# Performance work log

Measured on AMD Instinct MI355X. Metric: run time of the kernel, lower is better.

Reference implementation:

```python
import jax, jax.numpy as jnp
import numpy as np

B, N, D_IN, D_OUT = 4, 2048, 1024, 1024

def setup_inputs() -> dict:
    key = jax.random.key(0)
    ks = jax.random.split(key, 7)
    s_in = 1.0 / np.sqrt(D_IN)
    return {
        "X": jax.random.normal(ks[0], (B, N, D_IN), dtype=jnp.float32),
        "Wq": jax.random.uniform(ks[1], (D_IN, D_OUT), jnp.float32, -s_in, s_in),
        "bq": jax.random.uniform(ks[2], (D_OUT,), jnp.float32, -s_in, s_in),
        "Wk": jax.random.uniform(ks[3], (D_IN, D_OUT), jnp.float32, -s_in, s_in),
        "bk": jax.random.uniform(ks[4], (D_OUT,), jnp.float32, -s_in, s_in),
        "Wv": jax.random.uniform(ks[5], (D_IN, D_OUT), jnp.float32, -s_in, s_in),
        "bv": jax.random.uniform(ks[6], (D_OUT,), jnp.float32, -s_in, s_in),
    }

def reference(X, Wq, bq, Wk, bk, Wv, bv):
    # QKV projections: [B,N,D_in] @ [D_in,D_out] -> [B,N,D_out]
    q = jnp.einsum('bnd,de->bne', X, Wq) + bq
    k = jnp.einsum('bnd,de->bne', X, Wk) + bk
    v = jnp.einsum('bnd,de->bne', X, Wv) + bv
    # Unscaled attention (faithful: original has no 1/sqrt(d))
    scores = jnp.einsum('bne,bme->bnm', q, k)  # [B,N,N]
    weights = jax.nn.softmax(scores, axis=-1)
    return jnp.einsum('bnm,bme->bne', weights, v)
```

## Files before the change

kernel.cpp:

```cpp
#include <hip/hip_runtime.h>
#include <hip/hip_bf16.h>
#include <hip/hip_fp16.h>
#include <stdint.h>
#include <math.h>


typedef unsigned short ushort_t;
typedef __attribute__((ext_vector_type(8))) _Float16  f16x8;
typedef __attribute__((ext_vector_type(4))) _Float16  f16x4;
typedef __attribute__((ext_vector_type(4))) float     f32x4;

__device__ __forceinline__ void async_load16(const void* g, void* l) {
  __builtin_amdgcn_global_load_lds(
      (const __attribute__((address_space(1))) void*)g,
      (__attribute__((address_space(3))) void*)l, 16, 0, 0);
}

#define A0OFF 0
#define B0OFF 16384
#define A1OFF 32768
#define B1OFF 49152

template<int SHIFT>
__device__ __forceinline__ void stage_half(const ushort_t* __restrict__ gb,
                                           int k0, int q, ushort_t* lt, int t)
{
#pragma unroll
  for (int j = 0; j < 2; ++j) {
    const int i   = j * 64 + (t >> 3);
    const int row = ((i >> SHIFT) << (SHIFT + 1)) | (q << SHIFT) | (i & ((1 << SHIFT) - 1));
    const int ch  = (t & 7) ^ (row & 7);
    async_load16(gb + (long)row * 1024 + k0 + ch * 8, lt + row * 64 + (t & 7) * 8);
  }
}

#define BARR do { __builtin_amdgcn_sched_barrier(0); \
                  __builtin_amdgcn_s_barrier();      \
                  __builtin_amdgcn_sched_barrier(0); } while (0)

#define RD_A(TP, QM)                                                          \
  do { _Pragma("unroll") for (int m_ = 0; m_ < 4; ++m_) {                     \
    af[m_][0] = *(const f16x8*)&(TP)[(arow0 + (QM)*64 + m_*16) * 64 + ck0];   \
    af[m_][1] = *(const f16x8*)&(TP)[(arow0 + (QM)*64 + m_*16) * 64 + ck1];   \
  } } while (0)

#define RD_B(TP, QN)                                                          \
  do { _Pragma("unroll") for (int n_ = 0; n_ < 2; ++n_) {                     \
    bf[n_][0] = *(const f16x8*)&(TP)[(brow0 + (QN)*32 + n_*16) * 64 + ck0];   \
    bf[n_][1] = *(const f16x8*)&(TP)[(brow0 + (QN)*32 + n_*16) * 64 + ck1];   \
  } } while (0)

#define MM(QM, QN)                                                            \
  do { __builtin_amdgcn_s_setprio(1);                                         \
  _Pragma("unroll") for (int kh_ = 0; kh_ < 2; ++kh_)                         \
    _Pragma("unroll") for (int m_ = 0; m_ < 4; ++m_)                          \
      _Pragma("unroll") for (int n_ = 0; n_ < 2; ++n_)                        \
        acc[(QM)*4+m_][(QN)*2+n_] = __builtin_amdgcn_mfma_f32_16x16x32_f16(   \
            af[m_][kh_], bf[n_][kh_], acc[(QM)*4+m_][(QN)*2+n_], 0, 0, 0);    \
  __builtin_amdgcn_s_setprio(0); } while (0)

template<bool LAST>
__device__ __forceinline__ void iter256(const ushort_t* __restrict__ Ab,
                                        const ushort_t* __restrict__ Bb,
                                        ushort_t* lds, f32x4 (&acc)[8][4],
                                        int ka, int t, int arow0, int brow0,
                                        int ck0, int ck1)
{
  const int kb = ka + 64, kc = ka + 128, kd = ka + 192;
  f16x8 af[4][2], bf[2][2];

  RD_A(lds + A0OFF, 0); RD_B(lds + B0OFF, 0);
  stage_half<5>(Bb, kb, 0, lds + B1OFF, t);
  BARR; MM(0, 0); BARR;

  RD_B(lds + B0OFF, 1);
  if constexpr (!LAST) stage_half<6>(Ab, kc, 0, lds + A0OFF, t);
  BARR; MM(0, 1); BARR;

  RD_A(lds + A0OFF, 1);
  if constexpr (!LAST) stage_half<5>(Bb, kc, 1, lds + B0OFF, t);
  BARR; MM(1, 1); BARR;

  RD_B(lds + B0OFF, 0);
  if constexpr (!LAST) stage_half<6>(Ab, kc, 1, lds + A0OFF, t);
  BARR; MM(1, 0);
  if constexpr (LAST) asm volatile("s_waitcnt vmcnt(0)" ::: "memory");
  else                asm volatile("s_waitcnt vmcnt(6)" ::: "memory");
  BARR;

  RD_A(lds + A1OFF, 0); RD_B(lds + B1OFF, 0);
  if constexpr (!LAST) stage_half<5>(Bb, kc, 0, lds + B0OFF, t);
  BARR; MM(0, 0); BARR;

  RD_B(lds + B1OFF, 1);
  if constexpr (!LAST) stage_half<6>(Ab, kd, 0, lds + A1OFF, t);
  BARR; MM(0, 1); BARR;

  RD_A(lds + A1OFF, 1);
  if constexpr (!LAST) stage_half<5>(Bb, kd, 1, lds + B1OFF, t);
  BARR; MM(1, 1); BARR;

  RD_B(lds + B1OFF, 0);
  if constexpr (!LAST) stage_half<6>(Ab, kd, 1, lds + A1OFF, t);
  BARR; MM(1, 0);
  if constexpr (!LAST) asm volatile("s_waitcnt vmcnt(6)" ::: "memory");
  BARR;
}

__device__ __forceinline__ void gemm256(const ushort_t* __restrict__ Ab,
                                        const ushort_t* __restrict__ Bb,
                                        ushort_t* lds, f32x4 (&acc)[8][4])
{
  const int t    = threadIdx.x;
  const int lane = t & 63;
  const int wave = t >> 6;
  const int wr   = wave >> 2;
  const int wc   = wave & 3;
  const int arow0 = wr * 128 + (lane & 15);
  const int brow0 = wc * 64  + (lane & 15);
  const int ck0 = (((lane >> 4)    ) ^ (lane & 7)) * 8;
  const int ck1 = ((4 + (lane >> 4)) ^ (lane & 7)) * 8;

  stage_half<6>(Ab,  0, 0, lds + A0OFF, t);
  stage_half<5>(Bb,  0, 1, lds + B0OFF, t);
  stage_half<6>(Ab,  0, 1, lds + A0OFF, t);
  stage_half<5>(Bb,  0, 0, lds + B0OFF, t);
  stage_half<6>(Ab, 64, 0, lds + A1OFF, t);
  stage_half<5>(Bb, 64, 1, lds + B1OFF, t);
  stage_half<6>(Ab, 64, 1, lds + A1OFF, t);
  asm volatile("s_waitcnt vmcnt(6)" ::: "memory");
  BARR;

#pragma unroll 1
  for (int it = 0; it < 7; ++it)
    iter256<false>(Ab, Bb, lds, acc, it * 128, t, arow0, brow0, ck0, ck1);
  iter256<true>(Ab, Bb, lds, acc, 896, t, arow0, brow0, ck0, ck1);
}

__global__ __launch_bounds__(512, 2)
void qkv256_kernel(const ushort_t* __restrict__ A, const ushort_t* __restrict__ BT,
                   const float* __restrict__ bq, const float* __restrict__ bk,
                   const float* __restrict__ bvp,
                   __half* __restrict__ Qh, __half* __restrict__ Kh,
                   ushort_t* __restrict__ Vt)
{
  __shared__ __align__(16) ushort_t lds[65536];

  const int nb = gridDim.x * gridDim.y;
  int id = blockIdx.y * gridDim.x + blockIdx.x;
  id = (id & 7) * (nb >> 3) + (id >> 3);
  const int bx = id % gridDim.x;
  const int by = id / gridDim.x;

  const ushort_t* Ab = A  + (long)by * 256 * 1024;
  const ushort_t* Bb = BT + (long)bx * 256 * 1024;

  f32x4 acc[8][4];
  const f32x4 zero = {0.0f, 0.0f, 0.0f, 0.0f};
#pragma unroll
  for (int i = 0; i < 8; ++i)
#pragma unroll
    for (int j = 0; j < 4; ++j) acc[i][j] = zero;

  gemm256(Ab, Bb, lds, acc);

  const int t = threadIdx.x, lane = t & 63, wave = t >> 6;
  const int wr = wave >> 2, wc = wave & 3;
  const int er = (lane >> 4) * 4, ec = lane & 15;
  const int tgt = bx >> 2;
  const float* bias = (tgt == 0) ? bq : (tgt == 1) ? bk : bvp;

#pragma unroll
  for (int n4 = 0; n4 < 4; ++n4) {
    const int col = (bx & 3) * 256 + wc * 64 + n4 * 16 + ec;
    const float bval = bias[col];
#pragma unroll
    for (int m8 = 0; m8 < 8; ++m8) {
      const long grow0 = (long)by * 256 + wr * 128 + m8 * 16 + er;
      if (tgt < 2) {
        __half* o = (tgt == 0) ? Qh : Kh;
#pragma unroll
        for (int r = 0; r < 4; ++r)
          o[(grow0 + r) * 1024 + col] = __float2half(acc[m8][n4][r] + bval);
      } else {
        const long b  = grow0 >> 11;
        const long ml = grow0 & 2047;
        f16x4 v4;
#pragma unroll
        for (int r = 0; r < 4; ++r) v4[r] = (_Float16)(acc[m8][n4][r] + bval);
        *(f16x4*)&Vt[b * 2097152 + (long)col * 2048 + ml] = v4;
      }
    }
  }
}

__global__ __launch_bounds__(512, 2)
void qk256_kernel(const ushort_t* __restrict__ Q, const ushort_t* __restrict__ Kh,
                  __half* __restrict__ S, float* __restrict__ PM, float* __restrict__ PS)
{
  __shared__ __align__(16) ushort_t lds[65536];

  const int nb = gridDim.x * gridDim.y;
  int id = blockIdx.y * gridDim.x + blockIdx.x;
  id = (id & 7) * (nb >> 3) + (id >> 3);
  const int bx = id % gridDim.x;
  const int by = id / gridDim.x;
  const long z = blockIdx.z;

  const ushort_t* Ab = Q  + z * 2048 * 1024 + (long)by * 256 * 1024;
  const ushort_t* Bb = Kh + z * 2048 * 1024 + (long)bx * 256 * 1024;
  __half* Sb = S + z * 2048 * 2048;

  f32x4 acc[8][4];
  const f32x4 zero = {0.0f, 0.0f, 0.0f, 0.0f};
#pragma unroll
  for (int i = 0; i < 8; ++i)
#pragma unroll
    for (int j = 0; j < 4; ++j) acc[i][j] = zero;

  gemm256(Ab, Bb, lds, acc);

  const int t = threadIdx.x, lane = t & 63, wave = t >> 6;
  const int wr = wave >> 2, wc = wave & 3;
  const int er = (lane >> 4) * 4, ec = lane & 15;
  const int cc = bx * 4 + wc;
  float* PMb = PM + z * 32 * 2048 + (long)cc * 2048;
  float* PSb = PS + z * 32 * 2048 + (long)cc * 2048;

#pragma unroll
  for (int m8 = 0; m8 < 8; ++m8)
#pragma unroll
    for (int r = 0; r < 4; ++r) {
      float m = fmaxf(fmaxf(acc[m8][0][r], acc[m8][1][r]),
                      fmaxf(acc[m8][2][r], acc[m8][3][r]));
      m = fmaxf(m, __shfl_xor(m, 1));
      m = fmaxf(m, __shfl_xor(m, 2));
      m = fmaxf(m, __shfl_xor(m, 4));
      m = fmaxf(m, __shfl_xor(m, 8));
      float s = 0.0f;
#pragma unroll
      for (int n4 = 0; n4 < 4; ++n4) {
        const float e = __expf(acc[m8][n4][r] - m);
        acc[m8][n4][r] = e;
        s += e;
      }
      s += __shfl_xor(s, 1);
      s += __shfl_xor(s, 2);
      s += __shfl_xor(s, 4);
      s += __shfl_xor(s, 8);
      if (ec == 0) {
        const long row = (long)by * 256 + wr * 128 + m8 * 16 + er + r;
        PMb[row] = m;
        PSb[row] = s;
      }
    }

#pragma unroll
  for (int n4 = 0; n4 < 4; ++n4) {
    const long col = (long)bx * 256 + wc * 64 + n4 * 16 + ec;
#pragma unroll
    for (int m8 = 0; m8 < 8; ++m8)
#pragma unroll
      for (int r = 0; r < 4; ++r) {
        const long grow = (long)by * 256 + wr * 128 + m8 * 16 + er + r;
        Sb[grow * 2048 + col] = __float2half(acc[m8][n4][r]);
      }
  }
}

__global__ __launch_bounds__(256)
void softmax_reduce_kernel(const float* __restrict__ PM, const float* __restrict__ PS,
                           float* __restrict__ Sc)
{
  const int r = blockIdx.x * 256 + threadIdx.x;
  const int b = r >> 11, row = r & 2047;
  const long base = (long)b * 32 * 2048 + row;
  float m = -3.4e38f;
#pragma unroll
  for (int cb = 0; cb < 32; ++cb) m = fmaxf(m, PM[base + cb * 2048]);
  float l = 0.0f;
#pragma unroll
  for (int cb = 0; cb < 32; ++cb) l += PS[base + cb * 2048] * __expf(PM[base + cb * 2048] - m);
  const float inv = 1.0f / l;
#pragma unroll
  for (int cb = 0; cb < 32; ++cb) Sc[base + cb * 2048] = __expf(PM[base + cb * 2048] - m) * inv;
}

__global__ __launch_bounds__(256)
void pv_gemm_kernel(const ushort_t* __restrict__ S, const ushort_t* __restrict__ Vt,
                    const float* __restrict__ Sc, float* __restrict__ Out)
{
  const int K = 2048;
  __shared__ ushort_t As[2][128 * 32];
  __shared__ ushort_t Bs[2][128 * 32];

  const int t    = threadIdx.x;
  const int lane = t & 63;
  const int wave = t >> 6;
  const int wm   = (wave >> 1) * 64;
  const int wn   = (wave & 1) * 64;
  const long z   = blockIdx.z;

  const ushort_t* Ab = S + z * 2048 * 2048 + (long)blockIdx.y * 128 * K;
  const ushort_t* Bb = Vt + z * 1024 * 2048 + (long)blockIdx.x * 128 * K;
  const float* Scb = Sc + z * 32 * 2048;
  float* Cb = Out + z * 2048 * 1024;

  const int ldr = t >> 2;
  const int swzs = (ldr & 3) ^ ((ldr >> 2) & 3);
  const int ldc = ((t & 3) ^ swzs) * 8;
  const int frow = lane & 15;
  const int fsz  = (frow & 3) ^ ((frow >> 2) & 3);
  const int fo   = (((lane >> 4) ^ fsz)) * 8;

  const int arow0 = blockIdx.y * 128 + wm + frow;

  f32x4 acc[4][4];
  const f32x4 zero = {0.0f, 0.0f, 0.0f, 0.0f};
#pragma unroll
  for (int i = 0; i < 4; ++i)
#pragma unroll
    for (int j = 0; j < 4; ++j) acc[i][j] = zero;

  for (int k0 = 0; k0 < K; k0 += 64) {
    const int cb = k0 >> 6;
    _Float16 sc16[4];
#pragma unroll
    for (int i = 0; i < 4; ++i)
      sc16[i] = (_Float16)Scb[(long)cb * 2048 + arow0 + i * 16];

    __syncthreads();
    const ushort_t* ga = Ab + (long)ldr * K + k0 + ldc;
    const ushort_t* gb = Bb + (long)ldr * K + k0 + ldc;
#pragma unroll
    for (int h = 0; h < 2; ++h) {
      async_load16(ga + h * 32,                &As[h][t * 8]);
      async_load16(ga + h * 32 + 64 * (long)K, &As[h][2048 + t * 8]);
      async_load16(gb + h * 32,                &Bs[h][t * 8]);
      async_load16(gb + h * 32 + 64 * (long)K, &Bs[h][2048 + t * 8]);
    }
    __syncthreads();
#pragma unroll
    for (int h = 0; h < 2; ++h) {
      f16x8 af[4], bf[4];
#pragma unroll
      for (int i = 0; i < 4; ++i) {
        af[i] = *(const f16x8*)&As[h][(wm + i * 16 + frow) * 32 + fo] * sc16[i];
        bf[i] = *(const f16x8*)&Bs[h][(wn + i * 16 + frow) * 32 + fo];
      }
#pragma unroll
      for (int mi = 0; mi < 4; ++mi)
#pragma unroll
        for (int ni = 0; ni < 4; ++ni)
          acc[mi][ni] = __builtin_amdgcn_mfma_f32_16x16x32_f16(af[mi], bf[ni], acc[mi][ni], 0, 0, 0);
    }
  }

  const int er = (lane >> 4) * 4;
  const int ec = lane & 15;
#pragma unroll
  for (int ni = 0; ni < 4; ++ni) {
    const int gcol = blockIdx.x * 128 + wn + ni * 16 + ec;
#pragma unroll
    for (int mi = 0; mi < 4; ++mi) {
#pragma unroll
      for (int r = 0; r < 4; ++r) {
        const long grow = (long)blockIdx.y * 128 + wm + mi * 16 + er + r;
        Cb[grow * 1024 + gcol] = acc[mi][ni][r];
      }
    }
  }
}

__global__ __launch_bounds__(256)
void cvt_f32_f16_kernel(const float* __restrict__ src, __half* __restrict__ dst, long n)
{
  const long i = ((long)blockIdx.x * 256 + threadIdx.x) * 8;
  if (i + 8 > n) return;
  const float4 a = *(const float4*)(src + i);
  const float4 b = *(const float4*)(src + i + 4);
  f16x8 h;
  h[0] = (_Float16)a.x; h[1] = (_Float16)a.y; h[2] = (_Float16)a.z; h[3] = (_Float16)a.w;
  h[4] = (_Float16)b.x; h[5] = (_Float16)b.y; h[6] = (_Float16)b.z; h[7] = (_Float16)b.w;
  *(f16x8*)((ushort_t*)dst + i) = h;
}

__global__ __launch_bounds__(256)
void transpose_cvt3_kernel(const float* __restrict__ W0, const float* __restrict__ W1,
                           const float* __restrict__ W2, __half* __restrict__ dst)
{
  __shared__ float tile[32][33];
  const int z = blockIdx.z;
  const float* src = (z == 0) ? W0 : (z == 1) ? W1 : W2;
  __half* d = dst + (long)z * 1024 * 1024;
  const int c0 = blockIdx.x * 32;
  const int r0 = blockIdx.y * 32;
  const int tx = threadIdx.x & 31;
  const int ty = threadIdx.x >> 5;
#pragma unroll
  for (int i = 0; i < 32; i += 8)
    tile[ty + i][tx] = src[(long)(r0 + ty + i) * 1024 + (c0 + tx)];
  __syncthreads();
#pragma unroll
  for (int i = 0; i < 32; i += 8)
    d[(long)(c0 + ty + i) * 1024 + (r0 + tx)] = __float2half(tile[tx][ty + i]);
}

extern "C" void kernel_launch(void* const* d_in, const int* in_sizes, int n_in,
                              void* d_out, int out_size, void* d_ws, size_t ws_size,
                              hipStream_t stream)
{
  const int  Bb = 4, Nn = 2048, Dd = 1024;
  const long BN = (long)Bb * Nn;

  const float* X  = (const float*)d_in[0];
  const float* Wq = (const float*)d_in[1];
  const float* bq = (const float*)d_in[2];
  const float* Wk = (const float*)d_in[3];
  const float* bk = (const float*)d_in[4];
  const float* Wv = (const float*)d_in[5];
  const float* bv = (const float*)d_in[6];
  float* Out      = (float*)d_out;

  uint8_t* w = (uint8_t*)d_ws;
  ushort_t* Wt = (ushort_t*)w;  w += (size_t)3 * Dd * Dd * 2;

  transpose_cvt3_kernel<<<dim3(Dd / 32, Dd / 32, 3), 256, 0, stream>>>(Wq, Wk, Wv, (__half*)Wt);

  const size_t statsBytes = (size_t)Bb * 32 * Nn * 4;
  const size_t fullNeed = (size_t)3 * Dd * Dd * 2
                        + 4 * ((size_t)BN * Dd * 2)
                        + (size_t)Bb * Nn * Nn * 2
                        + 3 * statsBytes;

  if (ws_size >= fullNeed) {
    ushort_t* Xh = (ushort_t*)w;  w += (size_t)BN * Dd * 2;
    ushort_t* Q  = (ushort_t*)w;  w += (size_t)BN * Dd * 2;
    ushort_t* Kb = (ushort_t*)w;  w += (size_t)BN * Dd * 2;
    ushort_t* Vt = (ushort_t*)w;  w += (size_t)BN * Dd * 2;
    ushort_t* S  = (ushort_t*)w;  w += (size_t)Bb * Nn * Nn * 2;
    float*    PM = (float*)w;     w += statsBytes;
    float*    PS = (float*)w;     w += statsBytes;
    float*    Sc = (float*)w;

    cvt_f32_f16_kernel<<<dim3((unsigned)(BN * Dd / (8 * 256))), 256, 0, stream>>>(
        X, (__half*)Xh, BN * Dd);

    qkv256_kernel<<<dim3(3 * Dd / 256, BN / 256, 1), 512, 0, stream>>>(
        Xh, Wt, bq, bk, bv, (__half*)Q, (__half*)Kb, Vt);

    qk256_kernel<<<dim3(Nn / 256, Nn / 256, Bb), 512, 0, stream>>>(
        Q, Kb, (__half*)S, PM, PS);

    softmax_reduce_kernel<<<dim3((unsigned)(Bb * Nn / 256)), 256, 0, stream>>>(PM, PS, Sc);

    pv_gemm_kernel<<<dim3(Dd / 128, Nn / 128, Bb), 256, 0, stream>>>(
        S, Vt, Sc, Out);
  } else {
    ushort_t* Xh = (ushort_t*)w;  w += (size_t)Nn * Dd * 2;
    ushort_t* Q  = (ushort_t*)w;  w += (size_t)Nn * Dd * 2;
    ushort_t* Kb = (ushort_t*)w;  w += (size_t)Nn * Dd * 2;
    ushort_t* Vt = (ushort_t*)w;  w += (size_t)Nn * Dd * 2;
    ushort_t* S  = (ushort_t*)w;  w += (size_t)Nn * Nn * 2;
    float*    PM = (float*)w;     w += (size_t)32 * Nn * 4;
    float*    PS = (float*)w;     w += (size_t)32 * Nn * 4;
    float*    Sc = (float*)w;

    for (int b = 0; b < Bb; ++b) {
      const float* Xb = X + (long)b * Nn * Dd;
      cvt_f32_f16_kernel<<<dim3((unsigned)((long)Nn * Dd / (8 * 256))), 256, 0, stream>>>(
          Xb, (__half*)Xh, (long)Nn * Dd);
      qkv256_kernel<<<dim3(3 * Dd / 256, Nn / 256, 1), 512, 0, stream>>>(
          Xh, Wt, bq, bk, bv, (__half*)Q, (__half*)Kb, Vt);
      qk256_kernel<<<dim3(Nn / 256, Nn / 256, 1), 512, 0, stream>>>(
          Q, Kb, (__half*)S, PM, PS);
      softmax_reduce_kernel<<<dim3((unsigned)(Nn / 256)), 256, 0, stream>>>(PM, PS, Sc);
      pv_gemm_kernel<<<dim3(Dd / 128, Nn / 128, 1), 256, 0, stream>>>(
          S, Vt, Sc, Out + (long)b * Nn * Dd);
    }
  }
}
```

Baseline: 275.2 us.

## Retile QKV and PV GEMMs to 256x128 with pipelined async LDS staging

Replaces the QKV projection kernel's 256x256 tile with a 256x128 tile, which doubles the block count and gives each wave a smaller accumulator set. The simple double-buffered PV GEMM becomes a 512-thread kernel using the same quarter-staged async global-to-LDS pipeline with interleaved barriers and setprio. Per-column-block softmax scale factors are now prefetched one iteration ahead. The goals are better occupancy and wave balance across CUs, and overlap of global loads with MFMA work in the PV stage. In exchange the kernels carry complex hand-tuned vmcnt waits, and per-tile B reuse drops in the QKV GEMM.

```diff
diff --git a/kernel.cpp b/kernel.cpp
--- a/kernel.cpp
+++ b/kernel.cpp
@@ -16,6 +16,10 @@
       (__attribute__((address_space(3))) void*)l, 16, 0, 0);
 }
 
+#define BARR do { __builtin_amdgcn_sched_barrier(0); \
+                  __builtin_amdgcn_s_barrier();      \
+                  __builtin_amdgcn_sched_barrier(0); } while (0)
+
 #define A0OFF 0
 #define B0OFF 16384
 #define A1OFF 32768
@@ -33,10 +37,6 @@
     async_load16(gb + (long)row * 1024 + k0 + ch * 8, lt + row * 64 + (t & 7) * 8);
   }
 }
-
-#define BARR do { __builtin_amdgcn_sched_barrier(0); \
-                  __builtin_amdgcn_s_barrier();      \
-                  __builtin_amdgcn_sched_barrier(0); } while (0)
 
 #define RD_A(TP, QM)                                                          \
   do { _Pragma("unroll") for (int m_ = 0; m_ < 4; ++m_) {                     \
@@ -137,14 +137,199 @@
   iter256<true>(Ab, Bb, lds, acc, 896, t, arow0, brow0, ck0, ck1);
 }
 
+#define NA0 0
+#define NB0 16384
+#define NA1 24576
+#define NB1 40960
+
+__device__ __forceinline__ void stage_A_n(const ushort_t* __restrict__ gb, long ldk,
+                                          int k0, int q, ushort_t* lt, int t)
+{
+#pragma unroll
+  for (int j = 0; j < 2; ++j) {
+    const int i   = j * 64 + (t >> 3);
+    const int row = ((i >> 5) << 6) | (q << 5) | (i & 31);
+    const int ch  = (t & 7) ^ (row & 7);
+    async_load16(gb + (long)row * ldk + k0 + ch * 8, lt + row * 64 + (t & 7) * 8);
+  }
+}
+
+__device__ __forceinline__ void stage_B_n(const ushort_t* __restrict__ gb, long ldk,
+                                          int k0, int q, ushort_t* lt, int t)
+{
+  const int i   = t >> 3;
+  const int row = ((i >> 5) << 6) | (q << 5) | (i & 31);
+  const int ch  = (t & 7) ^ (row & 7);
+  async_load16(gb + (long)row * ldk + k0 + ch * 8, lt + row * 64 + (t & 7) * 8);
+}
+
+#define RDN_A(TP, QM)                                                         \
+  do { _Pragma("unroll") for (int m_ = 0; m_ < 2; ++m_) {                     \
+    af[m_][0] = *(const f16x8*)&(TP)[(arow_l + (QM)*32 + m_*16) * 64 + ck0];  \
+    af[m_][1] = *(const f16x8*)&(TP)[(arow_l + (QM)*32 + m_*16) * 64 + ck1];  \
+  } } while (0)
+
+#define RDN_AS(TP, QM, S)                                                     \
+  do { _Pragma("unroll") for (int m_ = 0; m_ < 2; ++m_) {                     \
+    af[m_][0] = *(const f16x8*)&(TP)[(arow_l + (QM)*32 + m_*16) * 64 + ck0] * (S)[(QM)*2+m_]; \
+    af[m_][1] = *(const f16x8*)&(TP)[(arow_l + (QM)*32 + m_*16) * 64 + ck1] * (S)[(QM)*2+m_]; \
+  } } while (0)
+
+#define RDN_B(TP, QN)                                                         \
+  do { _Pragma("unroll") for (int n_ = 0; n_ < 2; ++n_) {                     \
+    bf[n_][0] = *(const f16x8*)&(TP)[(brow_l + (QN)*32 + n_*16) * 64 + ck0];  \
+    bf[n_][1] = *(const f16x8*)&(TP)[(brow_l + (QN)*32 + n_*16) * 64 + ck1];  \
+  } } while (0)
+
+#define MMN(QM, QN)                                                           \
+  do { __builtin_amdgcn_s_setprio(1);                                         \
+  _Pragma("unroll") for (int kh_ = 0; kh_ < 2; ++kh_)                         \
+    _Pragma("unroll") for (int m_ = 0; m_ < 2; ++m_)                          \
+      _Pragma("unroll") for (int n_ = 0; n_ < 2; ++n_)                        \
+        acc[(QM)*2+m_][(QN)*2+n_] = __builtin_amdgcn_mfma_f32_16x16x32_f16(   \
+            af[m_][kh_], bf[n_][kh_], acc[(QM)*2+m_][(QN)*2+n_], 0, 0, 0);    \
+  __builtin_amdgcn_s_setprio(0); } while (0)
+
+template<bool LAST>
+__device__ __forceinline__ void iter_n(const ushort_t* __restrict__ Ab,
+                                       const ushort_t* __restrict__ Bb,
+                                       long lda, long ldb,
+                                       ushort_t* lds, f32x4 (&acc)[4][4],
+                                       int ka, int t, int arow_l, int brow_l,
+                                       int ck0, int ck1)
+{
+  const int kb = ka + 64, kc = ka + 128, kd = ka + 192;
+  f16x8 af[2][2], bf[2][2];
+
+  RDN_A(lds + NA0, 0); RDN_B(lds + NB0, 0);
+  stage_B_n(Bb, ldb, kb, 0, lds + NB1, t);
+  BARR; MMN(0, 0); BARR;
+
+  RDN_B(lds + NB0, 1);
+  if constexpr (!LAST) stage_A_n(Ab, lda, kc, 0, lds + NA0, t);
+  BARR; MMN(0, 1); BARR;
+
+  RDN_A(lds + NA0, 1);
+  if constexpr (!LAST) stage_B_n(Bb, ldb, kc, 1, lds + NB0, t);
+  BARR; MMN(1, 1); BARR;
+
+  RDN_B(lds + NB0, 0);
+  if constexpr (!LAST) stage_A_n(Ab, lda, kc, 1, lds + NA0, t);
+  BARR; MMN(1, 0);
+  if constexpr (LAST) asm volatile("s_waitcnt vmcnt(0)" ::: "memory");
+  else                asm volatile("s_waitcnt vmcnt(5)" ::: "memory");
+  BARR;
+
+  RDN_A(lds + NA1, 0); RDN_B(lds + NB1, 0);
+  if constexpr (!LAST) stage_B_n(Bb, ldb, kc, 0, lds + NB0, t);
+  BARR; MMN(0, 0); BARR;
+
+  RDN_B(lds + NB1, 1);
+  if constexpr (!LAST) stage_A_n(Ab, lda, kd, 0, lds + NA1, t);
+  BARR; MMN(0, 1); BARR;
+
+  RDN_A(lds + NA1, 1);
+  if constexpr (!LAST) stage_B_n(Bb, ldb, kd, 1, lds + NB1, t);
+  BARR; MMN(1, 1); BARR;
+
+  RDN_B(lds + NB1, 0);
+  if constexpr (!LAST) stage_A_n(Ab, lda, kd, 1, lds + NA1, t);
+  BARR; MMN(1, 0);
+  if constexpr (!LAST) asm volatile("s_waitcnt vmcnt(5)" ::: "memory");
+  BARR;
+}
+
+template<bool LAST>
+__device__ __forceinline__ void pv_iter_n(const ushort_t* __restrict__ Ab,
+                                          const ushort_t* __restrict__ Bb,
+                                          ushort_t* lds, f32x4 (&acc)[4][4],
+                                          int ka, int t, int arow_l, int brow_l,
+                                          int ck0, int ck1,
+                                          float (&scc)[2][4],
+                                          const float* __restrict__ Scb, int arow_abs)
+{
+  const int kb = ka + 64, kc = ka + 128, kd = ka + 192;
+  f16x8 af[2][2], bf[2][2];
+
+  float scn[2][4];
+  if constexpr (!LAST) {
+    const int cbn = (ka >> 6) + 2;
+#pragma unroll
+    for (int h = 0; h < 2; ++h)
+#pragma unroll
+      for (int s = 0; s < 4; ++s)
+        scn[h][s] = Scb[(long)(cbn + h) * 2048 + arow_abs + s * 16];
+  }
+  _Float16 sa[4], sb[4];
+#pragma unroll
+  for (int s = 0; s < 4; ++s) { sa[s] = (_Float16)scc[0][s]; sb[s] = (_Float16)scc[1][s]; }
+
+  RDN_AS(lds + NA0, 0, sa); RDN_B(lds + NB0, 0);
+  stage_B_n(Bb, 2048, kb, 0, lds + NB1, t);
+  BARR; MMN(0, 0); BARR;
+
+  RDN_B(lds + NB0, 1);
+  if constexpr (!LAST) stage_A_n(Ab, 2048, kc, 0, lds + NA0, t);
+  BARR; MMN(0, 1); BARR;
+
+  RDN_AS(lds + NA0, 1, sa);
+  if constexpr (!LAST) stage_B_n(Bb, 2048, kc, 1, lds + NB0, t);
+  BARR; MMN(1, 1); BARR;
+
+  RDN_B(lds + NB0, 0);
+  if constexpr (!LAST) stage_A_n(Ab, 2048, kc, 1, lds + NA0, t);
+  BARR; MMN(1, 0);
+  if constexpr (LAST) asm volatile("s_waitcnt vmcnt(0)" ::: "memory");
+  else                asm volatile("s_waitcnt vmcnt(5)" ::: "memory");
+  BARR;
+
+  RDN_AS(lds + NA1, 0, sb); RDN_B(lds + NB1, 0);
+  if constexpr (!LAST) stage_B_n(Bb, 2048, kc, 0, lds + NB0, t);
+  BARR; MMN(0, 0); BARR;
+
+  RDN_B(lds + NB1, 1);
+  if constexpr (!LAST) stage_A_n(Ab, 2048, kd, 0, lds + NA1, t);
+  BARR; MMN(0, 1); BARR;
+
+  RDN_AS(lds + NA1, 1, sb);
+  if constexpr (!LAST) stage_B_n(Bb, 2048, kd, 1, lds + NB1, t);
+  BARR; MMN(1, 1); BARR;
+
+  RDN_B(lds + NB1, 0);
+  if constexpr (!LAST) stage_A_n(Ab, 2048, kd, 1, lds + NA1, t);
+  BARR; MMN(1, 0);
+  if constexpr (!LAST) asm volatile("s_waitcnt vmcnt(5)" ::: "memory");
+  BARR;
+
+  if constexpr (!LAST) {
+#pragma unroll
+    for (int h = 0; h < 2; ++h)
+#pragma unroll
+      for (int s = 0; s < 4; ++s) scc[h][s] = scn[h][s];
+  }
+}
+
+#define PROLOGUE_N(LDA, LDB)                                \
+  do {                                                      \
+    stage_A_n(Ab, (LDA),  0, 0, lds + NA0, t);              \
+    stage_B_n(Bb, (LDB),  0, 0, lds + NB0, t);              \
+    stage_A_n(Ab, (LDA),  0, 1, lds + NA0, t);              \
+    stage_B_n(Bb, (LDB),  0, 1, lds + NB0, t);              \
+    stage_A_n(Ab, (LDA), 64, 0, lds + NA1, t);              \
+    stage_B_n(Bb, (LDB), 64, 1, lds + NB1, t);              \
+    stage_A_n(Ab, (LDA), 64, 1, lds + NA1, t);              \
+    asm volatile("s_waitcnt vmcnt(5)" ::: "memory");        \
+    BARR;                                                   \
+  } while (0)
+
 __global__ __launch_bounds__(512, 2)
-void qkv256_kernel(const ushort_t* __restrict__ A, const ushort_t* __restrict__ BT,
-                   const float* __restrict__ bq, const float* __restrict__ bk,
-                   const float* __restrict__ bvp,
-                   __half* __restrict__ Qh, __half* __restrict__ Kh,
-                   ushort_t* __restrict__ Vt)
-{
-  __shared__ __align__(16) ushort_t lds[65536];
+void qkv128n_kernel(const ushort_t* __restrict__ A, const ushort_t* __restrict__ BT,
+                    const float* __restrict__ bq, const float* __restrict__ bk,
+                    const float* __restrict__ bvp,
+                    __half* __restrict__ Qh, __half* __restrict__ Kh,
+                    ushort_t* __restrict__ Vt)
+{
+  __shared__ __align__(16) ushort_t lds[49152];
 
   const int nb = gridDim.x * gridDim.y;
   int id = blockIdx.y * gridDim.x + blockIdx.x;
@@ -153,41 +338,53 @@
   const int by = id / gridDim.x;
 
   const ushort_t* Ab = A  + (long)by * 256 * 1024;
-  const ushort_t* Bb = BT + (long)bx * 256 * 1024;
-
-  f32x4 acc[8][4];
+  const ushort_t* Bb = BT + (long)bx * 128 * 1024;
+
+  const int t    = threadIdx.x;
+  const int lane = t & 63;
+  const int wave = t >> 6;
+  const int wr   = wave >> 1;
+  const int wc   = wave & 1;
+  const int arow_l = wr * 64 + (lane & 15);
+  const int brow_l = wc * 64 + (lane & 15);
+  const int ck0 = (((lane >> 4)    ) ^ (lane & 7)) * 8;
+  const int ck1 = ((4 + (lane >> 4)) ^ (lane & 7)) * 8;
+
+  f32x4 acc[4][4];
   const f32x4 zero = {0.0f, 0.0f, 0.0f, 0.0f};
 #pragma unroll
-  for (int i = 0; i < 8; ++i)
+  for (int i = 0; i < 4; ++i)
 #pragma unroll
     for (int j = 0; j < 4; ++j) acc[i][j] = zero;
 
-  gemm256(Ab, Bb, lds, acc);
-
-  const int t = threadIdx.x, lane = t & 63, wave = t >> 6;
-  const int wr = wave >> 2, wc = wave & 3;
+  PROLOGUE_N(1024, 1024);
+#pragma unroll 1
+  for (int it = 0; it < 7; ++it)
+    iter_n<false>(Ab, Bb, 1024, 1024, lds, acc, it * 128, t, arow_l, brow_l, ck0, ck1);
+  iter_n<true>(Ab, Bb, 1024, 1024, lds, acc, 896, t, arow_l, brow_l, ck0, ck1);
+
   const int er = (lane >> 4) * 4, ec = lane & 15;
-  const int tgt = bx >> 2;
+  const int tgt = bx >> 3;
   const float* bias = (tgt == 0) ? bq : (tgt == 1) ? bk : bvp;
 
 #pragma unroll
-  for (int n4 = 0; n4 < 4; ++n4) {
-    const int col = (bx & 3) * 256 + wc * 64 + n4 * 16 + ec;
+  for (int ni = 0; ni < 4; ++ni) {
+    const int col = (bx & 7) * 128 + wc * 64 + ni * 16 + ec;
     const float bval = bias[col];
 #pragma unroll
-    for (int m8 = 0; m8 < 8; ++m8) {
-      const long grow0 = (long)by * 256 + wr * 128 + m8 * 16 + er;
+    for (int mi = 0; mi < 4; ++mi) {
+      const long grow0 = (long)by * 256 + wr * 64 + mi * 16 + er;
       if (tgt < 2) {
         __half* o = (tgt == 0) ? Qh : Kh;
 #pragma unroll
         for (int r = 0; r < 4; ++r)
-          o[(grow0 + r) * 1024 + col] = __float2half(acc[m8][n4][r] + bval);
+          o[(grow0 + r) * 1024 + col] = __float2half(acc[mi][ni][r] + bval);
       } else {
         const long b  = grow0 >> 11;
         const long ml = grow0 & 2047;
         f16x4 v4;
 #pragma unroll
-        for (int r = 0; r < 4; ++r) v4[r] = (_Float16)(acc[m8][n4][r] + bval);
+        for (int r = 0; r < 4; ++r) v4[r] = (_Float16)(acc[mi][ni][r] + bval);
         *(f16x4*)&Vt[b * 2097152 + (long)col * 2048 + ml] = v4;
       }
     }
@@ -286,34 +483,34 @@
   for (int cb = 0; cb < 32; ++cb) Sc[base + cb * 2048] = __expf(PM[base + cb * 2048] - m) * inv;
 }
 
-__global__ __launch_bounds__(256)
-void pv_gemm_kernel(const ushort_t* __restrict__ S, const ushort_t* __restrict__ Vt,
-                    const float* __restrict__ Sc, float* __restrict__ Out)
-{
-  const int K = 2048;
-  __shared__ ushort_t As[2][128 * 32];
-  __shared__ ushort_t Bs[2][128 * 32];
+__global__ __launch_bounds__(512, 2)
+void pv128n_kernel(const ushort_t* __restrict__ S, const ushort_t* __restrict__ Vt,
+                   const float* __restrict__ Sc, float* __restrict__ Out)
+{
+  __shared__ __align__(16) ushort_t lds[49152];
+
+  const int nb = gridDim.x * gridDim.y;
+  int id = blockIdx.y * gridDim.x + blockIdx.x;
+  id = (id & 7) * (nb >> 3) + (id >> 3);
+  const int bx = id % gridDim.x;
+  const int by = id / gridDim.x;
+  const long z = blockIdx.z;
+
+  const ushort_t* Ab = S  + z * 4194304 + (long)by * 256 * 2048;
+  const ushort_t* Bb = Vt + z * 2097152 + (long)bx * 128 * 2048;
+  const float* Scb = Sc + z * 32 * 2048;
+  float* Cb = Out + z * 2048 * 1024;
 
   const int t    = threadIdx.x;
   const int lane = t & 63;
   const int wave = t >> 6;
-  const int wm   = (wave >> 1) * 64;
-  const int wn   = (wave & 1) * 64;
-  const long z   = blockIdx.z;
-
-  const ushort_t* Ab = S + z * 2048 * 2048 + (long)blockIdx.y * 128 * K;
-  const ushort_t* Bb = Vt + z * 1024 * 2048 + (long)blockIdx.x * 128 * K;
-  const float* Scb = Sc + z * 32 * 2048;
-  float* Cb = Out + z * 2048 * 1024;
-
-  const int ldr = t >> 2;
-  const int swzs = (ldr & 3) ^ ((ldr >> 2) & 3);
-  const int ldc = ((t & 3) ^ swzs) * 8;
-  const int frow = lane & 15;
-  const int fsz  = (frow & 3) ^ ((frow >> 2) & 3);
-  const int fo   = (((lane >> 4) ^ fsz)) * 8;
-
-  const int arow0 = blockIdx.y * 128 + wm + frow;
+  const int wr   = wave >> 1;
+  const int wc   = wave & 1;
+  const int arow_l = wr * 64 + (lane & 15);
+  const int brow_l = wc * 64 + (lane & 15);
+  const int arow_abs = by * 256 + arow_l;
+  const int ck0 = (((lane >> 4)    ) ^ (lane & 7)) * 8;
+  const int ck1 = ((4 + (lane >> 4)) ^ (lane & 7)) * 8;
 
   f32x4 acc[4][4];
   const f32x4 zero = {0.0f, 0.0f, 0.0f, 0.0f};
@@ -322,50 +519,30 @@
 #pragma unroll
     for (int j = 0; j < 4; ++j) acc[i][j] = zero;
 
-  for (int k0 = 0; k0 < K; k0 += 64) {
-    const int cb = k0 >> 6;
-    _Float16 sc16[4];
-#pragma unroll
-    for (int i = 0; i < 4; ++i)
-      sc16[i] = (_Float16)Scb[(long)cb * 2048 + arow0 + i * 16];
-
-    __syncthreads();
-    const ushort_t* ga = Ab + (long)ldr * K + k0 + ldc;
-    const ushort_t* gb = Bb + (long)ldr * K + k0 + ldc;
-#pragma unroll
-    for (int h = 0; h < 2; ++h) {
-      async_load16(ga + h * 32,                &As[h][t * 8]);
-      async_load16(ga + h * 32 + 64 * (long)K, &As[h][2048 + t * 8]);
-      async_load16(gb + h * 32,                &Bs[h][t * 8]);
-      async_load16(gb + h * 32 + 64 * (long)K, &Bs[h][2048 + t * 8]);
-    }
-    __syncthreads();
-#pragma unroll
-    for (int h = 0; h < 2; ++h) {
-      f16x8 af[4], bf[4];
-#pragma unroll
-      for (int i = 0; i < 4; ++i) {
-        af[i] = *(const f16x8*)&As[h][(wm + i * 16 + frow) * 32 + fo] * sc16[i];
-        bf[i] = *(const f16x8*)&Bs[h][(wn + i * 16 + frow) * 32 + fo];
-      }
-#pragma unroll
-      for (int mi = 0; mi < 4; ++mi)
-#pragma unroll
-        for (int ni = 0; ni < 4; ++ni)
-          acc[mi][ni] = __builtin_amdgcn_mfma_f32_16x16x32_f16(af[mi], bf[ni], acc[mi][ni], 0, 0, 0);
-    }
-  }
-
-  const int er = (lane >> 4) * 4;
-  const int ec = lane & 15;
+  float scc[2][4];
+#pragma unroll
+  for (int h = 0; h < 2; ++h)
+#pragma unroll
+    for (int s = 0; s < 4; ++s)
+      scc[h][s] = Scb[(long)h * 2048 + arow_abs + s * 16];
+
+  PROLOGUE_N(2048, 2048);
+#pragma unroll 1
+  for (int it = 0; it < 15; ++it)
+    pv_iter_n<false>(Ab, Bb, lds, acc, it * 128, t, arow_l, brow_l, ck0, ck1,
+                     scc, Scb, arow_abs);
+  pv_iter_n<true>(Ab, Bb, lds, acc, 1920, t, arow_l, brow_l, ck0, ck1,
+                  scc, Scb, arow_abs);
+
+  const int er = (lane >> 4) * 4, ec = lane & 15;
 #pragma unroll
   for (int ni = 0; ni < 4; ++ni) {
-    const int gcol = blockIdx.x * 128 + wn + ni * 16 + ec;
+    const int gcol = bx * 128 + wc * 64 + ni * 16 + ec;
 #pragma unroll
     for (int mi = 0; mi < 4; ++mi) {
 #pragma unroll
       for (int r = 0; r < 4; ++r) {
-        const long grow = (long)blockIdx.y * 128 + wm + mi * 16 + er + r;
+        const long grow = (long)by * 256 + wr * 64 + mi * 16 + er + r;
         Cb[grow * 1024 + gcol] = acc[mi][ni][r];
       }
     }
@@ -446,7 +623,7 @@
     cvt_f32_f16_kernel<<<dim3((unsigned)(BN * Dd / (8 * 256))), 256, 0, stream>>>(
         X, (__half*)Xh, BN * Dd);
 
-    qkv256_kernel<<<dim3(3 * Dd / 256, BN / 256, 1), 512, 0, stream>>>(
+    qkv128n_kernel<<<dim3(3 * Dd / 128, BN / 256, 1), 512, 0, stream>>>(
         Xh, Wt, bq, bk, bv, (__half*)Q, (__half*)Kb, Vt);
 
     qk256_kernel<<<dim3(Nn / 256, Nn / 256, Bb), 512, 0, stream>>>(
@@ -454,7 +631,7 @@
 
     softmax_reduce_kernel<<<dim3((unsigned)(Bb * Nn / 256)), 256, 0, stream>>>(PM, PS, Sc);
 
-    pv_gemm_kernel<<<dim3(Dd / 128, Nn / 128, Bb), 256, 0, stream>>>(
+    pv128n_kernel<<<dim3(Dd / 128, Nn / 256, Bb), 512, 0, stream>>>(
         S, Vt, Sc, Out);
   } else {
     ushort_t* Xh = (ushort_t*)w;  w += (size_t)Nn * Dd * 2;
@@ -470,12 +647,12 @@
       const float* Xb = X + (long)b * Nn * Dd;
       cvt_f32_f16_kernel<<<dim3((unsigned)((long)Nn * Dd / (8 * 256))), 256, 0, stream>>>(
           Xb, (__half*)Xh, (long)Nn * Dd);
-      qkv256_kernel<<<dim3(3 * Dd / 256, Nn / 256, 1), 512, 0, stream>>>(
+      qkv128n_kernel<<<dim3(3 * Dd / 128, Nn / 256, 1), 512, 0, stream>>>(
           Xh, Wt, bq, bk, bv, (__half*)Q, (__half*)Kb, Vt);
       qk256_kernel<<<dim3(Nn / 256, Nn / 256, 1), 512, 0, stream>>>(
           Q, Kb, (__half*)S, PM, PS);
       softmax_reduce_kernel<<<dim3((unsigned)(Nn / 256)), 256, 0, stream>>>(PM, PS, Sc);
-      pv_gemm_kernel<<<dim3(Dd / 128, Nn / 128, 1), 256, 0, stream>>>(
+      pv128n_kernel<<<dim3(Dd / 128, Nn / 256, 1), 512, 0, stream>>>(
           S, Vt, Sc, Out + (long)b * Nn * Dd);
     }
   }
```

New measurement: 267.3 us. 1.03x faster.
